# Kernel tuning notes

Measured on AMD Instinct MI355X. Metric: run time of the kernel, lower is better.

Reference implementation:

```python
import jax, jax.numpy as jnp
import numpy as np

T, B, E, H = 200, 2048, 256, 512
P0, P1, NC = 256, 128, 1
ALPHA = 0.3  # keras LeakyReLU default


def _predict(h, W0, b0, W1, b1, Wf, bf):
    # Dense -> LeakyReLU -> (dropout=identity) x2, then sigmoid(Dense)
    h = jax.nn.leaky_relu(h @ W0 + b0, ALPHA)
    h = jax.nn.leaky_relu(h @ W1 + b1, ALPHA)
    return jax.nn.sigmoid(h @ Wf + bf)  # [B, 1]


def setup_inputs() -> dict:
    key = jax.random.key(0)
    ks = jax.random.split(key, 24)
    s = 0.05  # keras 'random_normal' initializer stddev
    d = {
        "inputs": jax.random.normal(ks[0], (T, B, E), jnp.float32),
        # gate order along leading axis: f, i, o, g
        "Wx_c": s * jax.random.normal(ks[1], (4, E, H), jnp.float32),
        "bx_c": jnp.zeros((4, H), jnp.float32),
        "Wh_c": s * jax.random.normal(ks[2], (4, H, H), jnp.float32),
        "Wx_v": s * jax.random.normal(ks[3], (4, E, H), jnp.float32),
        "bx_v": jnp.zeros((4, H), jnp.float32),
        "Wh_v": s * jax.random.normal(ks[4], (4, H, H), jnp.float32),
        # order: s_c_hat_c, s_c_hat_v, s_v_hat_v, s_v_hat_c
        "Ws": s * jax.random.normal(ks[5], (4, H, H), jnp.float32),
        "Wpc0": s * jax.random.normal(ks[6], (H, P0), jnp.float32),
        "bpc0": jnp.zeros((P0,), jnp.float32),
        "Wpc1": s * jax.random.normal(ks[7], (P0, P1), jnp.float32),
        "bpc1": jnp.zeros((P1,), jnp.float32),
        "Wfcc": s * jax.random.normal(ks[8], (P1, NC), jnp.float32),
        "bfcc": jnp.zeros((NC,), jnp.float32),
        "Wpv0": s * jax.random.normal(ks[9], (H, P0), jnp.float32),
        "bpv0": jnp.zeros((P0,), jnp.float32),
        "Wpv1": s * jax.random.normal(ks[10], (P0, P1), jnp.float32),
        "bpv1": jnp.zeros((P1,), jnp.float32),
        "Wfcv": s * jax.random.normal(ks[11], (P1, NC), jnp.float32),
        "bfcv": jnp.zeros((NC,), jnp.float32),
    }
    return d


def reference(inputs, Wx_c, bx_c, Wh_c, Wx_v, bx_v, Wh_v, Ws,
              Wpc0, bpc0, Wpc1, bpc1, Wfcc, bfcc,
              Wpv0, bpv0, Wpv1, bpv1, Wfcv, bfcv):
    batch = inputs.shape[1]
    zeros = jnp.zeros((batch, H), inputs.dtype)
    # initial g = predict_c(H_c=0), broadcast in place of tf.tile(g,[1,n_hidden])
    g0 = _predict(zeros, Wpc0, bpc0, Wpc1, bpc1, Wfcc, bfcc)  # [B,1]
    ones1 = jnp.ones_like(g0)

    def step(carry, x):
        H_c, H_v, s_c, s_v, g, pc, pv = carry
        # click stream gates: f,i,o,g fused along leading axis
        gx = jnp.einsum('be,keh->kbh', x, Wx_c) + bx_c[:, None, :]
        gh = jnp.einsum('bh,khg->kbg', H_c, Wh_c)
        pre = gx + gh
        f_c, i_c, o_c = jax.nn.sigmoid(pre[0]), jax.nn.sigmoid(pre[1]), jax.nn.sigmoid(pre[2])
        g_c = jnp.tanh(pre[3])
        s_c_hat = jnp.tanh((1.0 - g) * (H_c @ Ws[0]) + g * (H_v @ Ws[1]))
        s_c = s_c_hat + i_c * g_c + (1.0 - g) * (f_c * s_c)
        H_c = o_c * jnp.tanh(s_c)
        H_c_p = _predict(H_c, Wpc0, bpc0, Wpc1, bpc1, Wfcc, bfcc)  # [B,1]
        # no click_label branch: g = H_c_p
        g = H_c_p
        pc = jnp.where(H_c_p >= 0.5, ones1, (1.0 - H_c_p) * pc)
        # conversion stream gates (driven by updated H_c)
        gxv = jnp.einsum('be,keh->kbh', x, Wx_v) + bx_v[:, None, :]
        ghv = jnp.einsum('bh,khg->kbg', H_c, Wh_v)
        prev = gxv + ghv
        f_v, i_v, o_v = jax.nn.sigmoid(prev[0]), jax.nn.sigmoid(prev[1]), jax.nn.sigmoid(prev[2])
        g_v = jnp.tanh(prev[3])
        s_v_hat = jnp.tanh(H_v @ Ws[2] + g * (H_c @ Ws[3]))
        s_v = s_v_hat + (1.0 - g) * s_v + g * (f_v * s_v + i_v * g_v)
        H_v = (1.0 - g) * H_v + g * (o_v * jnp.tanh(s_v))
        H_v_p = _predict(H_v, Wpv0, bpv0, Wpv1, bpv1, Wfcv, bfcv) * H_c_p
        pv = jnp.where(H_c_p >= 0.5, ones1, (1.0 - H_v_p) * pv)
        return (H_c, H_v, s_c, s_v, g, pc, pv), (H_c_p, H_v_p)

    carry0 = (zeros, zeros, zeros, zeros, g0, ones1, ones1)
    _, (pred_c, pred_v) = jax.lax.scan(step, carry0, inputs)
    return pred_c, pred_v  # each [T, B, 1]
```

## Files before the change

### kernel.cpp

```cpp
#include <hip/hip_runtime.h>
#include <cstdint>
#include <cstddef>

constexpr int T_STEPS = 200;
constexpr int BATCH   = 2048;
constexpr int E_DIM   = 256;
constexpr int H_DIM   = 512;
constexpr int P0_DIM  = 256;
constexpr int P1_DIM  = 128;
constexpr float ALPHA = 0.3f;

typedef __attribute__((ext_vector_type(8))) _Float16 f16x8;
typedef __attribute__((ext_vector_type(4))) float f32x4;

__device__ __forceinline__ float sigmoidf_(float x){ return 1.0f/(1.0f+expf(-x)); }

__device__ __forceinline__ unsigned short f2h(float f){
    union { _Float16 h; unsigned short u; } v;
    v.h = (_Float16)f;
    return v.u;
}

#define GLOAD16(gp, lp) __builtin_amdgcn_global_load_lds( \
    (const __attribute__((address_space(1))) unsigned int*)(gp), \
    (__attribute__((address_space(3))) unsigned int*)(lp), 16, 0, 0)

template<int ROWS>
__device__ __forceinline__ void stage64(const unsigned short* __restrict__ src, int ldk,
                                        char* ldsbase){
    constexpr int TOT = ROWS * 8;
    const int tid = threadIdx.x;
#pragma unroll
    for (int i = 0; i < TOT/256; ++i){
        const int gsl = i*256 + tid;
        const int r = gsl >> 3, s = gsl & 7;
        const int ksrc = ((s ^ (r & 7)) << 3);
        GLOAD16(src + (size_t)r*ldk + ksrc, ldsbase + gsl*16);
    }
}

__device__ __forceinline__ f16x8 ldsfragh(const char* ldsbase, int row, int kslot){
    return *(const f16x8*)(ldsbase + row*128 + ((kslot ^ (row & 7)) << 4));
}

template<bool HAS_B1, bool HAS_B2, int KSLABS>
__device__ __forceinline__ void fused_phase(
    const unsigned short* __restrict__ A, int lda,
    const unsigned short* __restrict__ B1,
    const unsigned short* __restrict__ B2,
    f32x4 (&accg)[2][4], f32x4 (&acce)[2],
    char* lds, int wr, int wc, int lr, int lq)
{
    stage64<64>(A, lda, lds);
    if (HAS_B1) stage64<128>(B1, 768, lds + 8192);
    if (HAS_B2) stage64<32>(B2, 512, lds + 24576);
    int cur = 0;
    for (int s = 0; s < KSLABS; ++s){
        char* bufc = lds + cur*32768;
        if (s + 1 < KSLABS){
            char* bufn = lds + (cur^1)*32768;
            stage64<64>(A + (s+1)*64, lda, bufn);
            if (HAS_B1) stage64<128>(B1 + (s+1)*64, 768, bufn + 8192);
            if (HAS_B2) stage64<32>(B2 + (s+1)*64, 512, bufn + 24576);
            if constexpr (HAS_B1 && HAS_B2)
                asm volatile("s_waitcnt vmcnt(7)" ::: "memory");
            else if constexpr (HAS_B1)
                asm volatile("s_waitcnt vmcnt(6)" ::: "memory");
            else
                asm volatile("s_waitcnt vmcnt(3)" ::: "memory");
        } else {
            asm volatile("s_waitcnt vmcnt(0)" ::: "memory");
        }
        __builtin_amdgcn_s_barrier();
        __builtin_amdgcn_sched_barrier(0);
        __builtin_amdgcn_s_setprio(1);
#pragma unroll
        for (int kk = 0; kk < 2; ++kk){
            f16x8 a[2];
#pragma unroll
            for (int m = 0; m < 2; ++m) a[m] = ldsfragh(bufc, wr*32 + m*16 + lr, kk*4 + lq);
            if (HAS_B1){
#pragma unroll
                for (int n = 0; n < 4; ++n){
                    f16x8 b = ldsfragh(bufc + 8192, wc*64 + n*16 + lr, kk*4 + lq);
#pragma unroll
                    for (int m = 0; m < 2; ++m)
                        accg[m][n] = __builtin_amdgcn_mfma_f32_16x16x32_f16(a[m], b, accg[m][n], 0,0,0);
                }
            }
            if (HAS_B2){
                f16x8 b = ldsfragh(bufc + 24576, wc*16 + lr, kk*4 + lq);
#pragma unroll
                for (int m = 0; m < 2; ++m)
                    acce[m] = __builtin_amdgcn_mfma_f32_16x16x32_f16(a[m], b, acce[m], 0,0,0);
            }
        }
        __builtin_amdgcn_s_setprio(0);
        __builtin_amdgcn_sched_barrier(0);
        __builtin_amdgcn_s_barrier();
        cur ^= 1;
    }
}

__global__ __launch_bounds__(256, 2) void k_fused(
    const unsigned short* __restrict__ Xh,
    const unsigned short* __restrict__ AH,
    const unsigned short* __restrict__ AV,
    const unsigned short* __restrict__ WT2,
    const float* __restrict__ bias,
    const unsigned short* __restrict__ WsH,
    const unsigned short* __restrict__ WsV,
    const float* __restrict__ g,
    float* __restrict__ sstate, float* __restrict__ Hv32,
    unsigned short* __restrict__ Hnew,
    const int mode)
{
    __shared__ __align__(16) char lds[65536];
    const int tid = threadIdx.x;
    const int lane = tid & 63, wid = tid >> 6;
    const int wr = wid >> 1, wc = wid & 1;
    const int lr = lane & 15, lq = lane >> 4;

    const int id = blockIdx.x;
    const int virt = ((id & 7) << 6) | (id >> 3);
    const int hgrp = virt >> 5;
    const int brow = (virt & 31) * 64;
    const int h0   = hgrp * 32;

    f32x4 accg[2][4], acceH[2], acceV[2];
#pragma unroll
    for (int m = 0; m < 2; ++m){
        f32x4 z = {0.f,0.f,0.f,0.f};
#pragma unroll
        for (int n = 0; n < 4; ++n) accg[m][n] = z;
        acceH[m] = z; acceV[m] = z;
    }

    const unsigned short* WTp = WT2 + (size_t)hgrp*128*768;
    fused_phase<true,false,4>(Xh + (size_t)brow*E_DIM, E_DIM, WTp, nullptr,
                              accg, acceH, lds, wr, wc, lr, lq);
    fused_phase<true,true,8>(AH + (size_t)brow*H_DIM, H_DIM, WTp + E_DIM,
                             WsH + (size_t)h0*H_DIM,
                             accg, acceH, lds, wr, wc, lr, lq);
    fused_phase<false,true,8>(AV + (size_t)brow*H_DIM, H_DIM, nullptr,
                              WsV + (size_t)h0*H_DIM,
                              accg, acceV, lds, wr, wc, lr, lq);

    float* ldsG  = (float*)lds;
    float* ldsEH = (float*)(lds + 33792);
    float* ldsEV = (float*)(lds + 42240);
#pragma unroll
    for (int m = 0; m < 2; ++m){
#pragma unroll
        for (int n = 0; n < 4; ++n){
            const int col = wc*64 + n*16 + lr;
            const int z = col >> 5, hl = col & 31;
            const float bs = bias[z*H_DIM + h0 + hl];
#pragma unroll
            for (int r = 0; r < 4; ++r){
                const int row = wr*32 + m*16 + lq*4 + r;
                float v = accg[m][n][r] + bs;
                v = (z < 3) ? sigmoidf_(v) : tanhf(v);
                ldsG[row*132 + col] = v;
            }
        }
    }
#pragma unroll
    for (int m = 0; m < 2; ++m){
        const int col = wc*16 + lr;
#pragma unroll
        for (int r = 0; r < 4; ++r){
            const int row = wr*32 + m*16 + lq*4 + r;
            ldsEH[row*33 + col] = acceH[m][r];
            ldsEV[row*33 + col] = acceV[m][r];
        }
    }
    __syncthreads();

    const int crow = tid >> 2, ch = (tid & 3) * 8;
    const int grow = brow + crow;
    const float gv = g[grow];
    const size_t gbase = (size_t)grow*H_DIM + h0 + ch;
    union U4 { float4 v; float s[4]; };
    U4 sv0, sv1, hv0, hv1;
    sv0.v = *(const float4*)&sstate[gbase];
    sv1.v = *(const float4*)&sstate[gbase + 4];
    if (mode == 1){
        hv0.v = *(const float4*)&Hv32[gbase];
        hv1.v = *(const float4*)&Hv32[gbase + 4];
    }
    U4 sn0, sn1, hn0, hn1;
    union { unsigned short u[8]; f16x8 v; } hh;
#pragma unroll
    for (int e = 0; e < 8; ++e){
        const int hc = ch + e;
        const float f_ = ldsG[crow*132 + hc];
        const float i_ = ldsG[crow*132 + 32 + hc];
        const float o_ = ldsG[crow*132 + 64 + hc];
        const float q_ = ldsG[crow*132 + 96 + hc];
        const float eh = ldsEH[crow*33 + hc];
        const float ev = ldsEV[crow*33 + hc];
        const float a1 = (mode == 0) ? eh : ev;
        const float a2 = (mode == 0) ? ev : eh;
        const float svo = (e < 4) ? sv0.s[e] : sv1.s[e-4];
        float s, hval;
        if (mode == 0){
            const float shat = tanhf((1.0f - gv)*a1 + gv*a2);
            s = shat + i_*q_ + (1.0f - gv)*(f_*svo);
            hval = o_ * tanhf(s);
        } else {
            const float shat = tanhf(a1 + gv*a2);
            s = shat + (1.0f - gv)*svo + gv*(f_*svo + i_*q_);
            const float hvo = (e < 4) ? hv0.s[e] : hv1.s[e-4];
            hval = (1.0f - gv)*hvo + gv*(o_*tanhf(s));
            if (e < 4) hn0.s[e] = hval; else hn1.s[e-4] = hval;
        }
        if (e < 4) sn0.s[e] = s; else sn1.s[e-4] = s;
        hh.u[e] = f2h(hval);
    }
    *(float4*)&sstate[gbase]     = sn0.v;
    *(float4*)&sstate[gbase + 4] = sn1.v;
    if (mode == 1){
        *(float4*)&Hv32[gbase]     = hn0.v;
        *(float4*)&Hv32[gbase + 4] = hn1.v;
    }
    *(f16x8*)&Hnew[gbase] = hh.v;
}

__device__ __forceinline__ void predict_dev(
    int pblk, const unsigned short* __restrict__ Hh,
    const unsigned short* __restrict__ W0T, const float* __restrict__ b0,
    const unsigned short* __restrict__ W1T, const float* __restrict__ b1,
    const float* __restrict__ Wf, const float* __restrict__ bf_,
    float* gstate, const float* __restrict__ gmul, float* pred, char* lds)
{
    char*  ldsA = lds;
    char*  ldsB = lds + 4096;
    char*  ldsP = lds + 36864;
    float* sums = (float*)(lds + 53248);
    const int tid = threadIdx.x, lane = tid & 63, w = tid >> 6;
    const int lr = lane & 15, lq = lane >> 4;
    const int brow = pblk * 32;

    f32x4 acc0[2][4];
#pragma unroll
    for (int m = 0; m < 2; ++m)
#pragma unroll
        for (int n = 0; n < 4; ++n){ f32x4 z = {0.f,0.f,0.f,0.f}; acc0[m][n] = z; }

    for (int k0 = 0; k0 < H_DIM; k0 += 64){
        stage64<32>(Hh + (size_t)brow*H_DIM + k0, H_DIM, ldsA);
        stage64<256>(W0T + k0, H_DIM, ldsB);
        __syncthreads();
#pragma unroll
        for (int kk = 0; kk < 2; ++kk){
            f16x8 a[2], b[4];
#pragma unroll
            for (int m = 0; m < 2; ++m) a[m] = ldsfragh(ldsA, m*16 + lr, kk*4 + lq);
#pragma unroll
            for (int n = 0; n < 4; ++n) b[n] = ldsfragh(ldsB, w*64 + n*16 + lr, kk*4 + lq);
#pragma unroll
            for (int m = 0; m < 2; ++m)
#pragma unroll
                for (int n = 0; n < 4; ++n)
                    acc0[m][n] = __builtin_amdgcn_mfma_f32_16x16x32_f16(a[m], b[n], acc0[m][n], 0,0,0);
        }
        __syncthreads();
    }
#pragma unroll
    for (int m = 0; m < 2; ++m){
#pragma unroll
        for (int n = 0; n < 4; ++n){
            const int col = w*64 + n*16 + lr;
            const float bs = b0[col];
#pragma unroll
            for (int r = 0; r < 4; ++r){
                const int row = m*16 + lq*4 + r;
                float x = acc0[m][n][r] + bs;
                x = (x > 0.0f) ? x : ALPHA*x;
                *(unsigned short*)(ldsP + row*512 + ((((col >> 3)) ^ (row & 7)) << 4) + (col & 7)*2) = f2h(x);
            }
        }
    }
    __syncthreads();

    f32x4 accp[2][2];
#pragma unroll
    for (int m = 0; m < 2; ++m)
#pragma unroll
        for (int n = 0; n < 2; ++n){ f32x4 z = {0.f,0.f,0.f,0.f}; accp[m][n] = z; }

    for (int k0 = 0; k0 < P0_DIM; k0 += 64){
        stage64<128>(W1T + k0, P0_DIM, ldsB);
        __syncthreads();
#pragma unroll
        for (int kk = 0; kk < 2; ++kk){
            f16x8 a[2], b[2];
#pragma unroll
            for (int m = 0; m < 2; ++m){
                const int row = m*16 + lr;
                const int slot = (k0 >> 3) + kk*4 + lq;
                a[m] = *(const f16x8*)(ldsP + row*512 + ((slot ^ (row & 7)) << 4));
            }
#pragma unroll
            for (int n = 0; n < 2; ++n) b[n] = ldsfragh(ldsB, w*32 + n*16 + lr, kk*4 + lq);
#pragma unroll
            for (int m = 0; m < 2; ++m)
#pragma unroll
                for (int n = 0; n < 2; ++n)
                    accp[m][n] = __builtin_amdgcn_mfma_f32_16x16x32_f16(a[m], b[n], accp[m][n], 0,0,0);
        }
        __syncthreads();
    }

    float part[8];
#pragma unroll
    for (int j = 0; j < 8; ++j) part[j] = 0.0f;
#pragma unroll
    for (int m = 0; m < 2; ++m){
#pragma unroll
        for (int n = 0; n < 2; ++n){
            const int col = w*32 + n*16 + lr;
            const float bs = b1[col], wf = Wf[col];
#pragma unroll
            for (int r = 0; r < 4; ++r){
                float x = accp[m][n][r] + bs;
                x = (x > 0.0f) ? x : ALPHA*x;
                part[m*4 + r] += x * wf;
            }
        }
    }
#pragma unroll
    for (int mask = 1; mask < 16; mask <<= 1)
#pragma unroll
        for (int j = 0; j < 8; ++j) part[j] += __shfl_xor(part[j], mask);
    if (lr == 0){
#pragma unroll
        for (int j = 0; j < 8; ++j){
            const int row = (j >> 2)*16 + lq*4 + (j & 3);
            sums[w*32 + row] = part[j];
        }
    }
    __syncthreads();
    if (tid < 32){
        float tot = sums[tid] + sums[32 + tid] + sums[64 + tid] + sums[96 + tid] + bf_[0];
        float val = sigmoidf_(tot);
        const int rowg = brow + tid;
        if (gmul)   val *= gmul[rowg];
        if (gstate) gstate[rowg] = val;
        if (pred)   pred[rowg]   = val;
    }
}

__device__ __forceinline__ void xcvt_dev(int blk, const float* __restrict__ x,
                                         unsigned short* __restrict__ oh)
{
    const int tid = threadIdx.x;
#pragma unroll
    for (int j = 0; j < 4; ++j){
        const int t = blk*256 + tid + j*32768;
        float4 v = ((const float4*)x)[t];
        ushort4 h;
        h.x = f2h(v.x); h.y = f2h(v.y); h.z = f2h(v.z); h.w = f2h(v.w);
        ((ushort4*)oh)[t] = h;
    }
}

__global__ __launch_bounds__(256) void k_LB(
    const unsigned short* __restrict__ Hcn,
    const unsigned short* __restrict__ Wp0Tc, const float* __restrict__ bpc0,
    const unsigned short* __restrict__ Wp1Tc, const float* __restrict__ bpc1,
    const float* __restrict__ Wfcc, const float* __restrict__ bfcc,
    float* __restrict__ gnew, float* __restrict__ predc,
    const unsigned short* __restrict__ Hvb,
    const unsigned short* __restrict__ Wp0Tv, const float* __restrict__ bpv0,
    const unsigned short* __restrict__ Wp1Tv, const float* __restrict__ bpv1,
    const float* __restrict__ Wfcv, const float* __restrict__ bfcv,
    const float* __restrict__ gold, float* __restrict__ predv,
    const float* __restrict__ xnext, unsigned short* __restrict__ Xnh)
{
    __shared__ __align__(16) char lds[53760];
    const int id = blockIdx.x;
    if (id < 64){
        predict_dev(id, Hcn, Wp0Tc, bpc0, Wp1Tc, bpc1, Wfcc, bfcc,
                    gnew, nullptr, predc, lds);
    } else if (id < 128){
        if (predv) predict_dev(id - 64, Hvb, Wp0Tv, bpv0, Wp1Tv, bpv1, Wfcv, bfcv,
                               nullptr, gold, predv, lds);
    } else {
        if (Xnh) xcvt_dev(id - 128, xnext, Xnh);
    }
}

__global__ __launch_bounds__(256) void k_predict_g(
    const unsigned short* __restrict__ Hh,
    const unsigned short* __restrict__ W0T, const float* __restrict__ b0,
    const unsigned short* __restrict__ W1T, const float* __restrict__ b1,
    const float* __restrict__ Wf, const float* __restrict__ bf_,
    float* gstate, const float* __restrict__ gmul, float* pred)
{
    __shared__ __align__(16) char lds[53760];
    predict_dev(blockIdx.x, Hh, W0T, b0, W1T, b1, Wf, bf_, gstate, gmul, pred, lds);
}

__global__ __launch_bounds__(256) void k_xcvt_g(const float* __restrict__ x,
                                                unsigned short* __restrict__ oh)
{
    xcvt_dev(blockIdx.x, x, oh);
}

__global__ __launch_bounds__(256) void k_wcat(const float* __restrict__ Wx,
                                              const float* __restrict__ Wh,
                                              unsigned short* __restrict__ oh){
    const int n = blockIdx.y;
    const int k = blockIdx.x*256 + threadIdx.x;
    const int z = (n >> 5) & 3;
    const int h = ((n >> 7) << 5) | (n & 31);
    float v = (k < 256) ? Wx[((size_t)z*E_DIM + k)*H_DIM + h]
                        : Wh[((size_t)z*H_DIM + (k - 256))*H_DIM + h];
    oh[(size_t)n*768 + k] = f2h(v);
}

__global__ __launch_bounds__(256) void k_trans(const float* __restrict__ in,
                                               unsigned short* __restrict__ oh,
                                               int K, int N){
    const int k = blockIdx.x*256 + threadIdx.x;
    const int n = blockIdx.y;
    if (k < K) oh[(size_t)n*K + k] = f2h(in[(size_t)k*N + n]);
}

__global__ __launch_bounds__(256) void k_init(float* __restrict__ sc, float* __restrict__ sv,
                                              float* __restrict__ hv32,
                                              unsigned short* __restrict__ hc0,
                                              unsigned short* __restrict__ hv0){
    const int i = blockIdx.x*256 + threadIdx.x;
    sc[i] = 0.0f; sv[i] = 0.0f; hv32[i] = 0.0f;
    hc0[i] = 0; hv0[i] = 0;
}

extern "C" void kernel_launch(void* const* d_in, const int* in_sizes, int n_in,
                              void* d_out, int out_size, void* d_ws, size_t ws_size,
                              hipStream_t stream)
{
    (void)in_sizes; (void)n_in; (void)out_size; (void)ws_size;

    const float* inputs = (const float*)d_in[0];
    const float* Wx_c   = (const float*)d_in[1];
    const float* bx_c   = (const float*)d_in[2];
    const float* Wh_c   = (const float*)d_in[3];
    const float* Wx_v   = (const float*)d_in[4];
    const float* bx_v   = (const float*)d_in[5];
    const float* Wh_v   = (const float*)d_in[6];
    const float* Ws     = (const float*)d_in[7];
    const float* Wpc0   = (const float*)d_in[8];
    const float* bpc0   = (const float*)d_in[9];
    const float* Wpc1   = (const float*)d_in[10];
    const float* bpc1   = (const float*)d_in[11];
    const float* Wfcc   = (const float*)d_in[12];
    const float* bfcc   = (const float*)d_in[13];
    const float* Wpv0   = (const float*)d_in[14];
    const float* bpv0   = (const float*)d_in[15];
    const float* Wpv1   = (const float*)d_in[16];
    const float* bpv1   = (const float*)d_in[17];
    const float* Wfcv   = (const float*)d_in[18];
    const float* bfcv   = (const float*)d_in[19];
    float* out = (float*)d_out;

    char* ws = (char*)d_ws;
    size_t off = 0;
    auto allocB = [&](size_t bytes) -> char* {
        char* p = ws + off;
        off = (off + bytes + 255) & ~(size_t)255;
        return p;
    };
    const size_t BH = (size_t)BATCH * H_DIM;
    const size_t BE = (size_t)BATCH * E_DIM;

    unsigned short* Xh[2];
    Xh[0] = (unsigned short*)allocB(BE*2);
    Xh[1] = (unsigned short*)allocB(BE*2);
    unsigned short* WT2c  = (unsigned short*)allocB((size_t)2048*768*2);
    unsigned short* WT2v  = (unsigned short*)allocB((size_t)2048*768*2);
    unsigned short* WsT   = (unsigned short*)allocB((size_t)4*H_DIM*H_DIM*2);
    unsigned short* Wp0Tc = (unsigned short*)allocB((size_t)P0_DIM*H_DIM*2);
    unsigned short* Wp0Tv = (unsigned short*)allocB((size_t)P0_DIM*H_DIM*2);
    unsigned short* Wp1Tc = (unsigned short*)allocB((size_t)P1_DIM*P0_DIM*2);
    unsigned short* Wp1Tv = (unsigned short*)allocB((size_t)P1_DIM*P0_DIM*2);
    unsigned short* Hc[2], *Hv[2];
    Hc[0] = (unsigned short*)allocB(BH*2);
    Hc[1] = (unsigned short*)allocB(BH*2);
    Hv[0] = (unsigned short*)allocB(BH*2);
    Hv[1] = (unsigned short*)allocB(BH*2);
    float* sc    = (float*)allocB(BH*4);
    float* sv    = (float*)allocB(BH*4);
    float* hv32  = (float*)allocB(BH*4);
    float* gbuf[2];
    gbuf[0] = (float*)allocB(BATCH*4);
    gbuf[1] = (float*)allocB(BATCH*4);

    const dim3 thr(256);
    const size_t HH = (size_t)H_DIM * H_DIM;

    k_wcat<<<dim3(3, 2048), thr, 0, stream>>>(Wx_c, Wh_c, WT2c);
    k_wcat<<<dim3(3, 2048), thr, 0, stream>>>(Wx_v, Wh_v, WT2v);
    for (int i = 0; i < 4; ++i)
        k_trans<<<dim3(2, 512), thr, 0, stream>>>(Ws + i*HH, WsT + i*HH, H_DIM, H_DIM);
    k_trans<<<dim3(2, 256), thr, 0, stream>>>(Wpc0, Wp0Tc, H_DIM, P0_DIM);
    k_trans<<<dim3(2, 256), thr, 0, stream>>>(Wpv0, Wp0Tv, H_DIM, P0_DIM);
    k_trans<<<dim3(1, 128), thr, 0, stream>>>(Wpc1, Wp1Tc, P0_DIM, P1_DIM);
    k_trans<<<dim3(1, 128), thr, 0, stream>>>(Wpv1, Wp1Tv, P0_DIM, P1_DIM);

    k_init<<<4096, thr, 0, stream>>>(sc, sv, hv32, Hc[0], Hv[0]);
    k_predict_g<<<64, thr, 0, stream>>>(Hc[0], Wp0Tc, bpc0, Wp1Tc, bpc1, Wfcc, bfcc,
                                        gbuf[0], nullptr, nullptr);
    k_xcvt_g<<<128, thr, 0, stream>>>(inputs, Xh[0]);

    for (int t = 0; t < T_STEPS; ++t){
        const int cur = t & 1, nxt = cur ^ 1;

        k_fused<<<512, thr, 0, stream>>>(Xh[cur], Hc[cur], Hv[cur],
                                         WT2c, bx_c,
                                         WsT + 0*HH,
                                         WsT + 1*HH,
                                         gbuf[cur], sc, nullptr, Hc[nxt], 0);

        k_LB<<<256, thr, 0, stream>>>(Hc[nxt], Wp0Tc, bpc0, Wp1Tc, bpc1, Wfcc, bfcc,
                                      gbuf[nxt], out + (size_t)t*BATCH,
                                      Hv[cur], Wp0Tv, bpv0, Wp1Tv, bpv1, Wfcv, bfcv,
                                      gbuf[cur],
                                      (t > 0) ? out + (size_t)(T_STEPS + t - 1)*BATCH
                                              : nullptr,
                                      inputs + (size_t)(t+1)*BE,
                                      (t + 1 < T_STEPS) ? Xh[nxt] : nullptr);

        k_fused<<<512, thr, 0, stream>>>(Xh[cur], Hc[nxt], Hv[cur],
                                         WT2v, bx_v,
                                         WsT + 3*HH,
                                         WsT + 2*HH,
                                         gbuf[nxt], sv, hv32, Hv[nxt], 1);
    }
    k_predict_g<<<64, thr, 0, stream>>>(Hv[0], Wp0Tv, bpv0, Wp1Tv, bpv1, Wfcv, bfcv,
                                        nullptr, gbuf[0],
                                        out + (size_t)(2*T_STEPS - 1)*BATCH);
}
```

Baseline: 10.47 ms.

## Store operands in MFMA fragment-native layout and load fragments directly from global

All activations (X, Hc, Hv) and weights are now stored pre-swizzled in MFMA fragment order, so each lane loads its f16x8 fragment straight from global memory with one coalesced 16-byte load. This removes the LDS staging, double-buffering, waitcnt and barriers from the GEMM phases of k_fused and predict_dev, and shrinks LDS use, which may raise occupancy. Weight-prep kernels are rewritten to emit the fragment layout, and the H output writes are permuted to match. The cost is that there is no LDS reuse of A and B tiles across waves, so redundant global/L2 traffic rises and the latency of the direct loads is no longer hidden by explicit prefetching.

```diff
diff --git a/kernel.cpp b/kernel.cpp
--- a/kernel.cpp
+++ b/kernel.cpp
@@ -21,101 +21,23 @@
     return v.u;
 }
 
-#define GLOAD16(gp, lp) __builtin_amdgcn_global_load_lds( \
-    (const __attribute__((address_space(1))) unsigned int*)(gp), \
-    (__attribute__((address_space(3))) unsigned int*)(lp), 16, 0, 0)
-
-template<int ROWS>
-__device__ __forceinline__ void stage64(const unsigned short* __restrict__ src, int ldk,
-                                        char* ldsbase){
-    constexpr int TOT = ROWS * 8;
-    const int tid = threadIdx.x;
-#pragma unroll
-    for (int i = 0; i < TOT/256; ++i){
-        const int gsl = i*256 + tid;
-        const int r = gsl >> 3, s = gsl & 7;
-        const int ksrc = ((s ^ (r & 7)) << 3);
-        GLOAD16(src + (size_t)r*ldk + ksrc, ldsbase + gsl*16);
-    }
-}
-
-__device__ __forceinline__ f16x8 ldsfragh(const char* ldsbase, int row, int kslot){
-    return *(const f16x8*)(ldsbase + row*128 + ((kslot ^ (row & 7)) << 4));
-}
-
-template<bool HAS_B1, bool HAS_B2, int KSLABS>
-__device__ __forceinline__ void fused_phase(
-    const unsigned short* __restrict__ A, int lda,
-    const unsigned short* __restrict__ B1,
-    const unsigned short* __restrict__ B2,
-    f32x4 (&accg)[2][4], f32x4 (&acce)[2],
-    char* lds, int wr, int wc, int lr, int lq)
-{
-    stage64<64>(A, lda, lds);
-    if (HAS_B1) stage64<128>(B1, 768, lds + 8192);
-    if (HAS_B2) stage64<32>(B2, 512, lds + 24576);
-    int cur = 0;
-    for (int s = 0; s < KSLABS; ++s){
-        char* bufc = lds + cur*32768;
-        if (s + 1 < KSLABS){
-            char* bufn = lds + (cur^1)*32768;
-            stage64<64>(A + (s+1)*64, lda, bufn);
-            if (HAS_B1) stage64<128>(B1 + (s+1)*64, 768, bufn + 8192);
-            if (HAS_B2) stage64<32>(B2 + (s+1)*64, 512, bufn + 24576);
-            if constexpr (HAS_B1 && HAS_B2)
-                asm volatile("s_waitcnt vmcnt(7)" ::: "memory");
-            else if constexpr (HAS_B1)
-                asm volatile("s_waitcnt vmcnt(6)" ::: "memory");
-            else
-                asm volatile("s_waitcnt vmcnt(3)" ::: "memory");
-        } else {
-            asm volatile("s_waitcnt vmcnt(0)" ::: "memory");
-        }
-        __builtin_amdgcn_s_barrier();
-        __builtin_amdgcn_sched_barrier(0);
-        __builtin_amdgcn_s_setprio(1);
-#pragma unroll
-        for (int kk = 0; kk < 2; ++kk){
-            f16x8 a[2];
-#pragma unroll
-            for (int m = 0; m < 2; ++m) a[m] = ldsfragh(bufc, wr*32 + m*16 + lr, kk*4 + lq);
-            if (HAS_B1){
-#pragma unroll
-                for (int n = 0; n < 4; ++n){
-                    f16x8 b = ldsfragh(bufc + 8192, wc*64 + n*16 + lr, kk*4 + lq);
-#pragma unroll
-                    for (int m = 0; m < 2; ++m)
-                        accg[m][n] = __builtin_amdgcn_mfma_f32_16x16x32_f16(a[m], b, accg[m][n], 0,0,0);
-                }
-            }
-            if (HAS_B2){
-                f16x8 b = ldsfragh(bufc + 24576, wc*16 + lr, kk*4 + lq);
-#pragma unroll
-                for (int m = 0; m < 2; ++m)
-                    acce[m] = __builtin_amdgcn_mfma_f32_16x16x32_f16(a[m], b, acce[m], 0,0,0);
-            }
-        }
-        __builtin_amdgcn_s_setprio(0);
-        __builtin_amdgcn_sched_barrier(0);
-        __builtin_amdgcn_s_barrier();
-        cur ^= 1;
-    }
-}
+#define AFRAG(p, rg, NKB, kb) (*(const f16x8*)((p) + (((size_t)(rg)*(NKB) + (kb))*64 + lane)*8))
+#define BFRAG(p, cg, NKB, kb) (*(const f16x8*)((p) + (((size_t)(cg)*(NKB) + (kb))*64 + lane)*8))
 
 __global__ __launch_bounds__(256, 2) void k_fused(
-    const unsigned short* __restrict__ Xh,
-    const unsigned short* __restrict__ AH,
-    const unsigned short* __restrict__ AV,
-    const unsigned short* __restrict__ WT2,
+    const unsigned short* __restrict__ Xf,
+    const unsigned short* __restrict__ AHf,
+    const unsigned short* __restrict__ AVf,
+    const unsigned short* __restrict__ Wgf,
     const float* __restrict__ bias,
-    const unsigned short* __restrict__ WsH,
-    const unsigned short* __restrict__ WsV,
+    const unsigned short* __restrict__ WsHf,
+    const unsigned short* __restrict__ WsVf,
     const float* __restrict__ g,
     float* __restrict__ sstate, float* __restrict__ Hv32,
-    unsigned short* __restrict__ Hnew,
+    unsigned short* __restrict__ Hnewf,
     const int mode)
 {
-    __shared__ __align__(16) char lds[65536];
+    __shared__ __align__(16) char lds[50688];
     const int tid = threadIdx.x;
     const int lane = tid & 63, wid = tid >> 6;
     const int wr = wid >> 1, wc = wid & 1;
@@ -126,6 +48,7 @@
     const int hgrp = virt >> 5;
     const int brow = (virt & 31) * 64;
     const int h0   = hgrp * 32;
+    const int rgb  = brow >> 4;
 
     f32x4 accg[2][4], acceH[2], acceV[2];
 #pragma unroll
@@ -136,15 +59,43 @@
         acceH[m] = z; acceV[m] = z;
     }
 
-    const unsigned short* WTp = WT2 + (size_t)hgrp*128*768;
-    fused_phase<true,false,4>(Xh + (size_t)brow*E_DIM, E_DIM, WTp, nullptr,
-                              accg, acceH, lds, wr, wc, lr, lq);
-    fused_phase<true,true,8>(AH + (size_t)brow*H_DIM, H_DIM, WTp + E_DIM,
-                             WsH + (size_t)h0*H_DIM,
-                             accg, acceH, lds, wr, wc, lr, lq);
-    fused_phase<false,true,8>(AV + (size_t)brow*H_DIM, H_DIM, nullptr,
-                              WsV + (size_t)h0*H_DIM,
-                              accg, acceV, lds, wr, wc, lr, lq);
+    for (int kb = 0; kb < 8; ++kb){
+        f16x8 a[2];
+#pragma unroll
+        for (int m = 0; m < 2; ++m) a[m] = AFRAG(Xf, rgb + wr*2 + m, 8, kb);
+#pragma unroll
+        for (int n = 0; n < 4; ++n){
+            f16x8 b = BFRAG(Wgf, hgrp*8 + wc*4 + n, 24, kb);
+#pragma unroll
+            for (int m = 0; m < 2; ++m)
+                accg[m][n] = __builtin_amdgcn_mfma_f32_16x16x32_f16(a[m], b, accg[m][n], 0,0,0);
+        }
+    }
+    for (int kb = 0; kb < 16; ++kb){
+        f16x8 a[2];
+#pragma unroll
+        for (int m = 0; m < 2; ++m) a[m] = AFRAG(AHf, rgb + wr*2 + m, 16, kb);
+#pragma unroll
+        for (int n = 0; n < 4; ++n){
+            f16x8 b = BFRAG(Wgf, hgrp*8 + wc*4 + n, 24, 8 + kb);
+#pragma unroll
+            for (int m = 0; m < 2; ++m)
+                accg[m][n] = __builtin_amdgcn_mfma_f32_16x16x32_f16(a[m], b, accg[m][n], 0,0,0);
+        }
+        f16x8 bx = BFRAG(WsHf, hgrp*2 + wc, 16, kb);
+#pragma unroll
+        for (int m = 0; m < 2; ++m)
+            acceH[m] = __builtin_amdgcn_mfma_f32_16x16x32_f16(a[m], bx, acceH[m], 0,0,0);
+    }
+    for (int kb = 0; kb < 16; ++kb){
+        f16x8 a[2];
+#pragma unroll
+        for (int m = 0; m < 2; ++m) a[m] = AFRAG(AVf, rgb + wr*2 + m, 16, kb);
+        f16x8 bx = BFRAG(WsVf, hgrp*2 + wc, 16, kb);
+#pragma unroll
+        for (int m = 0; m < 2; ++m)
+            acceV[m] = __builtin_amdgcn_mfma_f32_16x16x32_f16(a[m], bx, acceV[m], 0,0,0);
+    }
 
     float* ldsG  = (float*)lds;
     float* ldsEH = (float*)(lds + 33792);
@@ -177,7 +128,7 @@
     }
     __syncthreads();
 
-    const int crow = tid >> 2, ch = (tid & 3) * 8;
+    const int crow = tid >> 2, lqq = tid & 3, ch = lqq * 8;
     const int grow = brow + crow;
     const float gv = g[grow];
     const size_t gbase = (size_t)grow*H_DIM + h0 + ch;
@@ -224,23 +175,20 @@
         *(float4*)&Hv32[gbase]     = hn0.v;
         *(float4*)&Hv32[gbase + 4] = hn1.v;
     }
-    *(f16x8*)&Hnew[gbase] = hh.v;
+    *(f16x8*)(Hnewf + (((size_t)(grow >> 4)*16 + hgrp)*64 + lqq*16 + (grow & 15))*8) = hh.v;
 }
 
 __device__ __forceinline__ void predict_dev(
-    int pblk, const unsigned short* __restrict__ Hh,
-    const unsigned short* __restrict__ W0T, const float* __restrict__ b0,
-    const unsigned short* __restrict__ W1T, const float* __restrict__ b1,
+    int pblk, const unsigned short* __restrict__ Hf,
+    const unsigned short* __restrict__ W0f, const float* __restrict__ b0,
+    const unsigned short* __restrict__ W1f, const float* __restrict__ b1,
     const float* __restrict__ Wf, const float* __restrict__ bf_,
     float* gstate, const float* __restrict__ gmul, float* pred, char* lds)
 {
-    char*  ldsA = lds;
-    char*  ldsB = lds + 4096;
-    char*  ldsP = lds + 36864;
-    float* sums = (float*)(lds + 53248);
+    char*  ldsP = lds;
+    float* sums = (float*)(lds + 16384);
     const int tid = threadIdx.x, lane = tid & 63, w = tid >> 6;
     const int lr = lane & 15, lq = lane >> 4;
-    const int brow = pblk * 32;
 
     f32x4 acc0[2][4];
 #pragma unroll
@@ -248,24 +196,17 @@
 #pragma unroll
         for (int n = 0; n < 4; ++n){ f32x4 z = {0.f,0.f,0.f,0.f}; acc0[m][n] = z; }
 
-    for (int k0 = 0; k0 < H_DIM; k0 += 64){
-        stage64<32>(Hh + (size_t)brow*H_DIM + k0, H_DIM, ldsA);
-        stage64<256>(W0T + k0, H_DIM, ldsB);
-        __syncthreads();
-#pragma unroll
-        for (int kk = 0; kk < 2; ++kk){
-            f16x8 a[2], b[4];
-#pragma unroll
-            for (int m = 0; m < 2; ++m) a[m] = ldsfragh(ldsA, m*16 + lr, kk*4 + lq);
-#pragma unroll
-            for (int n = 0; n < 4; ++n) b[n] = ldsfragh(ldsB, w*64 + n*16 + lr, kk*4 + lq);
+    for (int kb = 0; kb < 16; ++kb){
+        f16x8 a[2];
+#pragma unroll
+        for (int m = 0; m < 2; ++m) a[m] = AFRAG(Hf, pblk*2 + m, 16, kb);
+#pragma unroll
+        for (int n = 0; n < 4; ++n){
+            f16x8 b = BFRAG(W0f, w*4 + n, 16, kb);
 #pragma unroll
             for (int m = 0; m < 2; ++m)
-#pragma unroll
-                for (int n = 0; n < 4; ++n)
-                    acc0[m][n] = __builtin_amdgcn_mfma_f32_16x16x32_f16(a[m], b[n], acc0[m][n], 0,0,0);
-        }
-        __syncthreads();
+                acc0[m][n] = __builtin_amdgcn_mfma_f32_16x16x32_f16(a[m], b, acc0[m][n], 0,0,0);
+        }
     }
 #pragma unroll
     for (int m = 0; m < 2; ++m){
@@ -273,12 +214,13 @@
         for (int n = 0; n < 4; ++n){
             const int col = w*64 + n*16 + lr;
             const float bs = b0[col];
+            const int kb2 = col >> 5, lq2 = (col >> 3) & 3, e2 = col & 7;
 #pragma unroll
             for (int r = 0; r < 4; ++r){
                 const int row = m*16 + lq*4 + r;
                 float x = acc0[m][n][r] + bs;
                 x = (x > 0.0f) ? x : ALPHA*x;
-                *(unsigned short*)(ldsP + row*512 + ((((col >> 3)) ^ (row & 7)) << 4) + (col & 7)*2) = f2h(x);
+                ((unsigned short*)ldsP)[((m*8 + kb2)*64 + lq2*16 + (row & 15))*8 + e2] = f2h(x);
             }
         }
     }
@@ -290,27 +232,18 @@
 #pragma unroll
         for (int n = 0; n < 2; ++n){ f32x4 z = {0.f,0.f,0.f,0.f}; accp[m][n] = z; }
 
-    for (int k0 = 0; k0 < P0_DIM; k0 += 64){
-        stage64<128>(W1T + k0, P0_DIM, ldsB);
-        __syncthreads();
-#pragma unroll
-        for (int kk = 0; kk < 2; ++kk){
-            f16x8 a[2], b[2];
-#pragma unroll
-            for (int m = 0; m < 2; ++m){
-                const int row = m*16 + lr;
-                const int slot = (k0 >> 3) + kk*4 + lq;
-                a[m] = *(const f16x8*)(ldsP + row*512 + ((slot ^ (row & 7)) << 4));
-            }
-#pragma unroll
-            for (int n = 0; n < 2; ++n) b[n] = ldsfragh(ldsB, w*32 + n*16 + lr, kk*4 + lq);
+    for (int kb = 0; kb < 8; ++kb){
+        f16x8 a[2];
+#pragma unroll
+        for (int m = 0; m < 2; ++m)
+            a[m] = *(const f16x8*)((unsigned short*)ldsP + (((m*8 + kb)*64 + lane))*8);
+#pragma unroll
+        for (int n = 0; n < 2; ++n){
+            f16x8 b = BFRAG(W1f, w*2 + n, 8, kb);
 #pragma unroll
             for (int m = 0; m < 2; ++m)
-#pragma unroll
-                for (int n = 0; n < 2; ++n)
-                    accp[m][n] = __builtin_amdgcn_mfma_f32_16x16x32_f16(a[m], b[n], accp[m][n], 0,0,0);
-        }
-        __syncthreads();
+                accp[m][n] = __builtin_amdgcn_mfma_f32_16x16x32_f16(a[m], b, accp[m][n], 0,0,0);
+        }
     }
 
     float part[8];
@@ -345,88 +278,126 @@
     if (tid < 32){
         float tot = sums[tid] + sums[32 + tid] + sums[64 + tid] + sums[96 + tid] + bf_[0];
         float val = sigmoidf_(tot);
-        const int rowg = brow + tid;
+        const int rowg = pblk*32 + tid;
         if (gmul)   val *= gmul[rowg];
         if (gstate) gstate[rowg] = val;
         if (pred)   pred[rowg]   = val;
     }
 }
 
-__device__ __forceinline__ void xcvt_dev(int blk, const float* __restrict__ x,
-                                         unsigned short* __restrict__ oh)
-{
-    const int tid = threadIdx.x;
-#pragma unroll
-    for (int j = 0; j < 4; ++j){
-        const int t = blk*256 + tid + j*32768;
-        float4 v = ((const float4*)x)[t];
-        ushort4 h;
-        h.x = f2h(v.x); h.y = f2h(v.y); h.z = f2h(v.z); h.w = f2h(v.w);
-        ((ushort4*)oh)[t] = h;
+__device__ __forceinline__ void xf_dev(int blk, const float* __restrict__ x,
+                                       unsigned short* __restrict__ Xf)
+{
+    const int t0 = blk*256 + threadIdx.x;
+#pragma unroll
+    for (int rep = 0; rep < 2; ++rep){
+        const int gch = t0 + rep*32768;
+        const int rg = gch >> 9, kb = (gch >> 6) & 7, ln = gch & 63;
+        const int lrr = ln & 15, lqq = ln >> 4;
+        const float* src = x + (size_t)(rg*16 + lrr)*E_DIM + kb*32 + lqq*8;
+        float4 v0 = *(const float4*)src, v1 = *(const float4*)(src + 4);
+        union { unsigned short u[8]; f16x8 v; } hh;
+        hh.u[0]=f2h(v0.x); hh.u[1]=f2h(v0.y); hh.u[2]=f2h(v0.z); hh.u[3]=f2h(v0.w);
+        hh.u[4]=f2h(v1.x); hh.u[5]=f2h(v1.y); hh.u[6]=f2h(v1.z); hh.u[7]=f2h(v1.w);
+        *(f16x8*)(Xf + (size_t)gch*8) = hh.v;
     }
 }
 
 __global__ __launch_bounds__(256) void k_LB(
-    const unsigned short* __restrict__ Hcn,
-    const unsigned short* __restrict__ Wp0Tc, const float* __restrict__ bpc0,
-    const unsigned short* __restrict__ Wp1Tc, const float* __restrict__ bpc1,
+    const unsigned short* __restrict__ Hcnf,
+    const unsigned short* __restrict__ W0fc, const float* __restrict__ bpc0,
+    const unsigned short* __restrict__ W1fc, const float* __restrict__ bpc1,
     const float* __restrict__ Wfcc, const float* __restrict__ bfcc,
     float* __restrict__ gnew, float* __restrict__ predc,
-    const unsigned short* __restrict__ Hvb,
-    const unsigned short* __restrict__ Wp0Tv, const float* __restrict__ bpv0,
-    const unsigned short* __restrict__ Wp1Tv, const float* __restrict__ bpv1,
+    const unsigned short* __restrict__ Hvbf,
+    const unsigned short* __restrict__ W0fv, const float* __restrict__ bpv0,
+    const unsigned short* __restrict__ W1fv, const float* __restrict__ bpv1,
     const float* __restrict__ Wfcv, const float* __restrict__ bfcv,
     const float* __restrict__ gold, float* __restrict__ predv,
-    const float* __restrict__ xnext, unsigned short* __restrict__ Xnh)
-{
-    __shared__ __align__(16) char lds[53760];
+    const float* __restrict__ xnext, unsigned short* __restrict__ Xnf)
+{
+    __shared__ __align__(16) char lds[16896];
     const int id = blockIdx.x;
     if (id < 64){
-        predict_dev(id, Hcn, Wp0Tc, bpc0, Wp1Tc, bpc1, Wfcc, bfcc,
+        predict_dev(id, Hcnf, W0fc, bpc0, W1fc, bpc1, Wfcc, bfcc,
                     gnew, nullptr, predc, lds);
     } else if (id < 128){
-        if (predv) predict_dev(id - 64, Hvb, Wp0Tv, bpv0, Wp1Tv, bpv1, Wfcv, bfcv,
+        if (predv) predict_dev(id - 64, Hvbf, W0fv, bpv0, W1fv, bpv1, Wfcv, bfcv,
                                nullptr, gold, predv, lds);
     } else {
-        if (Xnh) xcvt_dev(id - 128, xnext, Xnh);
+        if (Xnf) xf_dev(id - 128, xnext, Xnf);
     }
 }
 
 __global__ __launch_bounds__(256) void k_predict_g(
-    const unsigned short* __restrict__ Hh,
-    const unsigned short* __restrict__ W0T, const float* __restrict__ b0,
-    const unsigned short* __restrict__ W1T, const float* __restrict__ b1,
+    const unsigned short* __restrict__ Hf,
+    const unsigned short* __restrict__ W0f, const float* __restrict__ b0,
+    const unsigned short* __restrict__ W1f, const float* __restrict__ b1,
     const float* __restrict__ Wf, const float* __restrict__ bf_,
     float* gstate, const float* __restrict__ gmul, float* pred)
 {
-    __shared__ __align__(16) char lds[53760];
-    predict_dev(blockIdx.x, Hh, W0T, b0, W1T, b1, Wf, bf_, gstate, gmul, pred, lds);
-}
-
-__global__ __launch_bounds__(256) void k_xcvt_g(const float* __restrict__ x,
-                                                unsigned short* __restrict__ oh)
-{
-    xcvt_dev(blockIdx.x, x, oh);
-}
-
-__global__ __launch_bounds__(256) void k_wcat(const float* __restrict__ Wx,
-                                              const float* __restrict__ Wh,
-                                              unsigned short* __restrict__ oh){
-    const int n = blockIdx.y;
-    const int k = blockIdx.x*256 + threadIdx.x;
-    const int z = (n >> 5) & 3;
-    const int h = ((n >> 7) << 5) | (n & 31);
-    float v = (k < 256) ? Wx[((size_t)z*E_DIM + k)*H_DIM + h]
-                        : Wh[((size_t)z*H_DIM + (k - 256))*H_DIM + h];
-    oh[(size_t)n*768 + k] = f2h(v);
-}
-
-__global__ __launch_bounds__(256) void k_trans(const float* __restrict__ in,
-                                               unsigned short* __restrict__ oh,
-                                               int K, int N){
-    const int k = blockIdx.x*256 + threadIdx.x;
-    const int n = blockIdx.y;
-    if (k < K) oh[(size_t)n*K + k] = f2h(in[(size_t)k*N + n]);
+    __shared__ __align__(16) char lds[16896];
+    predict_dev(blockIdx.x, Hf, W0f, b0, W1f, b1, Wf, bf_, gstate, gmul, pred, lds);
+}
+
+__global__ __launch_bounds__(256) void k_xf_g(const float* __restrict__ x,
+                                              unsigned short* __restrict__ Xf)
+{
+    xf_dev(blockIdx.x, x, Xf);
+}
+
+__global__ __launch_bounds__(256) void k_wgf(const float* __restrict__ Wx,
+                                             const float* __restrict__ Wh,
+                                             unsigned short* __restrict__ out){
+    const int kbg = blockIdx.x, cg = blockIdx.y;
+    const int t = threadIdx.x;
+    const int ln = t >> 2, eq = (t & 3) * 2;
+    const int lrr = ln & 15, lqq = ln >> 4;
+    const int hgrp = cg >> 3, n16 = cg & 7;
+    const int col128 = n16*16 + lrr;
+    const int z = col128 >> 5, hl = col128 & 31;
+    const int h = hgrp*32 + hl;
+    const size_t off = (((size_t)cg*24 + kbg)*64 + ln)*8 + eq;
+#pragma unroll
+    for (int e = 0; e < 2; ++e){
+        const int k = kbg*32 + lqq*8 + eq + e;
+        const float v = (k < 256) ? Wx[((size_t)z*E_DIM + k)*H_DIM + h]
+                                  : Wh[((size_t)z*H_DIM + (k - 256))*H_DIM + h];
+        out[off + e] = f2h(v);
+    }
+}
+
+__global__ __launch_bounds__(256) void k_wsf(const float* __restrict__ Ws,
+                                             unsigned short* __restrict__ out){
+    const int kb = blockIdx.x, icg = blockIdx.y;
+    const int i = icg >> 5, cg = icg & 31;
+    const int t = threadIdx.x;
+    const int ln = t >> 2, eq = (t & 3) * 2;
+    const int lrr = ln & 15, lqq = ln >> 4;
+    const int col = cg*16 + lrr;
+    const size_t off = ((((size_t)i*32 + cg)*16 + kb)*64 + ln)*8 + eq;
+#pragma unroll
+    for (int e = 0; e < 2; ++e){
+        const int k = kb*32 + lqq*8 + eq + e;
+        out[off + e] = f2h(Ws[((size_t)i*H_DIM + k)*H_DIM + col]);
+    }
+}
+
+__global__ __launch_bounds__(256) void k_wpf(const float* __restrict__ W,
+                                             unsigned short* __restrict__ out,
+                                             int K, int N){
+    const int kb = blockIdx.x, cg = blockIdx.y;
+    const int t = threadIdx.x;
+    const int ln = t >> 2, eq = (t & 3) * 2;
+    const int lrr = ln & 15, lqq = ln >> 4;
+    const int col = cg*16 + lrr;
+    const int NKB = K >> 5;
+    const size_t off = (((size_t)cg*NKB + kb)*64 + ln)*8 + eq;
+#pragma unroll
+    for (int e = 0; e < 2; ++e){
+        const int k = kb*32 + lqq*8 + eq + e;
+        out[off + e] = f2h(W[(size_t)k*N + col]);
+    }
 }
 
 __global__ __launch_bounds__(256) void k_init(float* __restrict__ sc, float* __restrict__ sv,
@@ -476,21 +447,21 @@
     const size_t BH = (size_t)BATCH * H_DIM;
     const size_t BE = (size_t)BATCH * E_DIM;
 
-    unsigned short* Xh[2];
-    Xh[0] = (unsigned short*)allocB(BE*2);
-    Xh[1] = (unsigned short*)allocB(BE*2);
-    unsigned short* WT2c  = (unsigned short*)allocB((size_t)2048*768*2);
-    unsigned short* WT2v  = (unsigned short*)allocB((size_t)2048*768*2);
-    unsigned short* WsT   = (unsigned short*)allocB((size_t)4*H_DIM*H_DIM*2);
-    unsigned short* Wp0Tc = (unsigned short*)allocB((size_t)P0_DIM*H_DIM*2);
-    unsigned short* Wp0Tv = (unsigned short*)allocB((size_t)P0_DIM*H_DIM*2);
-    unsigned short* Wp1Tc = (unsigned short*)allocB((size_t)P1_DIM*P0_DIM*2);
-    unsigned short* Wp1Tv = (unsigned short*)allocB((size_t)P1_DIM*P0_DIM*2);
-    unsigned short* Hc[2], *Hv[2];
-    Hc[0] = (unsigned short*)allocB(BH*2);
-    Hc[1] = (unsigned short*)allocB(BH*2);
-    Hv[0] = (unsigned short*)allocB(BH*2);
-    Hv[1] = (unsigned short*)allocB(BH*2);
+    unsigned short* Xf[2];
+    Xf[0] = (unsigned short*)allocB(BE*2);
+    Xf[1] = (unsigned short*)allocB(BE*2);
+    unsigned short* Wgfc = (unsigned short*)allocB((size_t)128*24*64*8*2);
+    unsigned short* Wgfv = (unsigned short*)allocB((size_t)128*24*64*8*2);
+    unsigned short* Wsf  = (unsigned short*)allocB((size_t)4*32*16*64*8*2);
+    unsigned short* W0fc = (unsigned short*)allocB((size_t)16*16*64*8*2);
+    unsigned short* W0fv = (unsigned short*)allocB((size_t)16*16*64*8*2);
+    unsigned short* W1fc = (unsigned short*)allocB((size_t)8*8*64*8*2);
+    unsigned short* W1fv = (unsigned short*)allocB((size_t)8*8*64*8*2);
+    unsigned short* Hcf[2], *Hvf[2];
+    Hcf[0] = (unsigned short*)allocB(BH*2);
+    Hcf[1] = (unsigned short*)allocB(BH*2);
+    Hvf[0] = (unsigned short*)allocB(BH*2);
+    Hvf[1] = (unsigned short*)allocB(BH*2);
     float* sc    = (float*)allocB(BH*4);
     float* sv    = (float*)allocB(BH*4);
     float* hv32  = (float*)allocB(BH*4);
@@ -499,47 +470,46 @@
     gbuf[1] = (float*)allocB(BATCH*4);
 
     const dim3 thr(256);
-    const size_t HH = (size_t)H_DIM * H_DIM;
-
-    k_wcat<<<dim3(3, 2048), thr, 0, stream>>>(Wx_c, Wh_c, WT2c);
-    k_wcat<<<dim3(3, 2048), thr, 0, stream>>>(Wx_v, Wh_v, WT2v);
-    for (int i = 0; i < 4; ++i)
-        k_trans<<<dim3(2, 512), thr, 0, stream>>>(Ws + i*HH, WsT + i*HH, H_DIM, H_DIM);
-    k_trans<<<dim3(2, 256), thr, 0, stream>>>(Wpc0, Wp0Tc, H_DIM, P0_DIM);
-    k_trans<<<dim3(2, 256), thr, 0, stream>>>(Wpv0, Wp0Tv, H_DIM, P0_DIM);
-    k_trans<<<dim3(1, 128), thr, 0, stream>>>(Wpc1, Wp1Tc, P0_DIM, P1_DIM);
-    k_trans<<<dim3(1, 128), thr, 0, stream>>>(Wpv1, Wp1Tv, P0_DIM, P1_DIM);
-
-    k_init<<<4096, thr, 0, stream>>>(sc, sv, hv32, Hc[0], Hv[0]);
-    k_predict_g<<<64, thr, 0, stream>>>(Hc[0], Wp0Tc, bpc0, Wp1Tc, bpc1, Wfcc, bfcc,
+    const size_t WSFM = (size_t)32*16*64*8;
+
+    k_wgf<<<dim3(24, 128), thr, 0, stream>>>(Wx_c, Wh_c, Wgfc);
+    k_wgf<<<dim3(24, 128), thr, 0, stream>>>(Wx_v, Wh_v, Wgfv);
+    k_wsf<<<dim3(16, 128), thr, 0, stream>>>(Ws, Wsf);
+    k_wpf<<<dim3(16, 16), thr, 0, stream>>>(Wpc0, W0fc, H_DIM, P0_DIM);
+    k_wpf<<<dim3(16, 16), thr, 0, stream>>>(Wpv0, W0fv, H_DIM, P0_DIM);
+    k_wpf<<<dim3(8, 8),   thr, 0, stream>>>(Wpc1, W1fc, P0_DIM, P1_DIM);
+    k_wpf<<<dim3(8, 8),   thr, 0, stream>>>(Wpv1, W1fv, P0_DIM, P1_DIM);
+
+    k_init<<<4096, thr, 0, stream>>>(sc, sv, hv32, Hcf[0], Hvf[0]);
+    k_predict_g<<<64, thr, 0, stream>>>(Hcf[0], W0fc, bpc0, W1fc, bpc1, Wfcc, bfcc,
                                         gbuf[0], nullptr, nullptr);
-    k_xcvt_g<<<128, thr, 0, stream>>>(inputs, Xh[0]);
+    k_xf_g<<<128, thr, 0, stream>>>(inputs, Xf[0]);
 
     for (int t = 0; t < T_STEPS; ++t){
         const int cur = t & 1, nxt = cur ^ 1;
 
-        k_fused<<<512, thr, 0, stream>>>(Xh[cur], Hc[cur], Hv[cur],
-                                         WT2c, bx_c,
-                                         WsT + 0*HH,
-                                         WsT + 1*HH,
-                                         gbuf[cur], sc, nullptr, Hc[nxt], 0);
-
-        k_LB<<<256, thr, 0, stream>>>(Hc[nxt], Wp0Tc, bpc0, Wp1Tc, bpc1, Wfcc, bfcc,
+        k_fused<<<512, thr, 0, stream>>>(Xf[cur], Hcf[cur], Hvf[cur],
+                                         Wgfc, bx_c,
+                                         Wsf + 0*WSFM,
+                                         Wsf + 1*WSFM,
+                                         gbuf[cur], sc, nullptr, Hcf[nxt], 0);
+
+        k_LB<<<256, thr, 0, stream>>>(Hcf[nxt], W0fc, bpc0, W1fc, bpc1, Wfcc, bfcc,
                                       gbuf[nxt], out + (size_t)t*BATCH,
-                                      Hv[cur], Wp0Tv, bpv0, Wp1Tv, bpv1, Wfcv, bfcv,
+                                      Hvf[cur], W0fv, bpv0, W1fv, bpv1, Wfcv, bfcv,
                                       gbuf[cur],
                                       (t > 0) ? out + (size_t)(T_STEPS + t - 1)*BATCH
                                               : nullptr,
                                       inputs + (size_t)(t+1)*BE,
-                                      (t + 1 < T_STEPS) ? Xh[nxt] : nullptr);
-
-        k_fused<<<512, thr, 0, stream>>>(Xh[cur], Hc[nxt], Hv[cur],
-                                         WT2v, bx_v,
-                                         WsT + 3*HH,
-                                         WsT + 2*HH,
-                                         gbuf[nxt], sv, hv32, Hv[nxt], 1);
-    }
-    k_predict_g<<<64, thr, 0, stream>>>(Hv[0], Wp0Tv, bpv0, Wp1Tv, bpv1, Wfcv, bfcv,
+                                      (t + 1 < T_STEPS) ? Xf[nxt] : nullptr);
+
+        k_fused<<<512, thr, 0, stream>>>(Xf[cur], Hcf[nxt], Hvf[cur],
+                                         Wgfv, bx_v,
+                                         Wsf + 3*WSFM,
+                                         Wsf + 2*WSFM,
+                                         gbuf[nxt], sv, hv32, Hvf[nxt], 1);
+    }
+    k_predict_g<<<64, thr, 0, stream>>>(Hvf[0], W0fv, bpv0, W1fv, bpv1, Wfcv, bfcv,
                                         nullptr, gbuf[0],
                                         out + (size_t)(2*T_STEPS - 1)*BATCH);
 }
```

Result: slower. 15.90 ms (+51.8%).
